# Kernel tuning notes

Measured on AMD Instinct MI355X. Metric: run time of the kernel, lower is better.

The kernel has to match this reference:

```python
import jax, jax.numpy as jnp
import numpy as np

B, N, NV, RESO, C_LAT = 1, 16384, 6890, 256, 192
C3 = C_LAT // 3            # 64 channels per uv/uh/hv plane
N_FREQ = 10                # NeRF PE -> 3*(2*10+1) = 63
UVH_DIM = 3 * (2 * N_FREQ + 1)
VIEW_DIM = 27
DEPTH_BOUND = 0.1
RGB_DIM = 3


def _embed(p):
    # p [B,N,3] -> [B,N,63]  (identity + sin/cos at 2^i freqs)
    freqs = (2.0 ** jnp.arange(N_FREQ)).astype(p.dtype)
    ang = p[..., None] * freqs                      # [B,N,3,F]
    s = jnp.sin(ang).reshape(p.shape[0], p.shape[1], -1)
    c = jnp.cos(ang).reshape(p.shape[0], p.shape[1], -1)
    return jnp.concatenate([p, s, c], axis=-1)


def _bilinear(plane, uv):
    # plane [B,C,H,W], uv [B,N,2] in [0,1] -> [B,C,N] (align_corners=True, border clamp)
    Bp, C, H, W = plane.shape
    x = jnp.clip(uv[..., 0], 0.0, 1.0) * (W - 1)
    y = jnp.clip(uv[..., 1], 0.0, 1.0) * (H - 1)
    x0 = jnp.floor(x); y0 = jnp.floor(y)
    wx = (x - x0)[:, None, :]; wy = (y - y0)[:, None, :]
    x0i = jnp.clip(x0.astype(jnp.int32), 0, W - 1)
    x1i = jnp.clip(x0i + 1, 0, W - 1)
    y0i = jnp.clip(y0.astype(jnp.int32), 0, H - 1)
    y1i = jnp.clip(y0i + 1, 0, H - 1)
    flat = plane.reshape(Bp, C, H * W)
    def g(yi, xi):
        idx = (yi * W + xi)[:, None, :]
        return jnp.take_along_axis(flat, jnp.broadcast_to(idx, (Bp, C, idx.shape[-1])), axis=2)
    f00 = g(y0i, x0i); f01 = g(y0i, x1i); f10 = g(y1i, x0i); f11 = g(y1i, x1i)
    return (f00 * (1 - wx) * (1 - wy) + f01 * wx * (1 - wy)
            + f10 * (1 - wx) * wy + f11 * wx * wy)


def _conv1d(x, w, b):
    # 1x1 Conv1d == channel matmul: x [B,Cin,N], w [Cout,Cin]
    return jnp.einsum('oc,bcn->bon', w, x) + b[None, :, None]


def _forward(sampled_pts, smpl_vertices, view_dir, input_latent, vts_uv,
             w_geo0, b_geo0, w_geo1, b_geo1, w_alpha, b_alpha,
             w_view0, b_view0, w_view1, b_view1, w_rgb, b_rgb):
    # --- KNN (k=1) nearest SMPL vertex via gram trick (no [B,N,V,3] diff) ---
    p2 = jnp.sum(sampled_pts ** 2, -1)                     # [B,N]
    v2 = jnp.sum(smpl_vertices ** 2, -1)                   # [B,V]
    d2 = (p2[:, :, None] + v2[:, None, :]
          - 2.0 * jnp.einsum('bnd,bvd->bnv', sampled_pts, smpl_vertices))  # [B,N,V]
    idx = jnp.argmin(d2, axis=-1)                          # [B,N]
    h = jnp.sqrt(jnp.maximum(jnp.min(d2, axis=-1), 1e-12))[..., None]      # [B,N,1]
    near_uv = vts_uv[0][idx]                               # [B,N,2]

    # --- uvh positional encoding (before depth normalization) ---
    pts_huv = jnp.concatenate([h, near_uv], axis=2)        # [B,N,3]
    huvlat = _embed(pts_huv).transpose(0, 2, 1)            # [B,63,N]

    # --- tri-plane (uv / uh / hv) grid-sample lookups ---
    h_n = (h / DEPTH_BOUND + 1.0) / 2.0
    uv_pl = input_latent[:, :C3]
    uh_pl = input_latent[:, C3:2 * C3]
    hv_pl = input_latent[:, 2 * C3:]
    uh = jnp.concatenate([near_uv[..., :1], h_n], -1)
    hv = jnp.concatenate([h_n, near_uv[..., 1:]], -1)
    fused = (_bilinear(uv_pl, near_uv) + _bilinear(uh_pl, uh) + _bilinear(hv_pl, hv)) / 3.0  # [B,64,N]

    # --- NeRF head (1x1 Conv1d MLP) ---
    nerf_in = jnp.concatenate([fused, huvlat], 1)          # [B,127,N]
    net = jax.nn.relu(_conv1d(nerf_in, w_geo0, b_geo0))
    net = jax.nn.relu(_conv1d(net, w_geo1, b_geo1))
    alpha = _conv1d(net, w_alpha, b_alpha)                 # [B,1,N]
    feat = jnp.concatenate([net, view_dir.transpose(0, 2, 1), fused], 1)   # [B,347,N]
    net = jax.nn.relu(_conv1d(feat, w_view0, b_view0))
    net = jax.nn.relu(_conv1d(net, w_view1, b_view1))
    rgb = _conv1d(net, w_rgb, b_rgb)                       # [B,3,N]
    return jnp.concatenate([alpha, rgb], 1).transpose(0, 2, 1)  # [B,N,4]


def setup_inputs():
    key = jax.random.key(0)
    ks = jax.random.split(key, 12)
    def rn(k, shape, scale=1.0):
        return (jax.random.normal(k, shape) * scale).astype(jnp.float32)
    return {
        'sampled_pts': rn(ks[0], (B, N, 3), 0.3),
        'smpl_vertices': rn(ks[1], (B, NV, 3), 0.3),
        'view_dir': rn(ks[2], (B, N, VIEW_DIM)),
        'input_latent': rn(ks[3], (B, C_LAT, RESO, RESO), 0.1),
        'vts_uv': jax.random.uniform(ks[4], (1, NV, 2), dtype=jnp.float32),
        'w_geo0': rn(ks[5], (256, C3 + UVH_DIM), 0.05), 'b_geo0': jnp.zeros(256),
        'w_geo1': rn(ks[6], (256, 256), 0.05), 'b_geo1': jnp.zeros(256),
        'w_alpha': rn(ks[7], (1, 256), 0.05), 'b_alpha': jnp.zeros(1),
        'w_view0': rn(ks[8], (256, 256 + VIEW_DIM + C3), 0.05), 'b_view0': jnp.zeros(256),
        'w_view1': rn(ks[9], (128, 256), 0.05), 'b_view1': jnp.zeros(128),
        'w_rgb': rn(ks[10], (RGB_DIM, 128), 0.05), 'b_rgb': jnp.zeros(RGB_DIM),
    }


def reference(sampled_pts, smpl_vertices, view_dir, input_latent, vts_uv,
              w_geo0, b_geo0, w_geo1, b_geo1, w_alpha, b_alpha,
              w_view0, b_view0, w_view1, b_view1, w_rgb, b_rgb):
    return _forward(sampled_pts, smpl_vertices, view_dir, input_latent, vts_uv,
                    w_geo0, b_geo0, w_geo1, b_geo1, w_alpha, b_alpha,
                    w_view0, b_view0, w_view1, b_view1, w_rgb, b_rgb)
```

## Files before the change

### kernel.cpp

```cpp
#include <hip/hip_runtime.h>
#include <hip/hip_bf16.h>
#include <math.h>
#include <float.h>

#define N_PTS 16384
#define NVERT 6890
#define RESO 256
#define C_LAT 192
#define VIEW_DIM 27

#define NCHUNK 16
#define CHUNK 431

typedef __hip_bfloat16 bf16;
typedef __bf16 bf16x8 __attribute__((ext_vector_type(8)));
typedef float f32x4 __attribute__((ext_vector_type(4)));

__device__ __forceinline__ void gload_lds16(const void* g, void* l) {
    __builtin_amdgcn_global_load_lds(
        (const __attribute__((address_space(1))) unsigned int*)g,
        (__attribute__((address_space(3))) unsigned int*)l, 16, 0, 0);
}

__global__ __launch_bounds__(256) void transpose_latent(const float* __restrict__ lat,
                                                        bf16* __restrict__ latT) {
    __shared__ float tile[C_LAT][65];
    int b = blockIdx.x;
    int y = b >> 2;
    int x0 = (b & 3) << 6;
    int t = threadIdx.x;
    #pragma unroll
    for (int i = 0; i < (C_LAT * 64) / 256; ++i) {
        int e = i * 256 + t;
        int c = e >> 6, xi = e & 63;
        tile[c][xi] = lat[c * (RESO * RESO) + y * RESO + x0 + xi];
    }
    __syncthreads();
    #pragma unroll
    for (int i = 0; i < (C_LAT * 64) / 256; ++i) {
        int e = i * 256 + t;
        int xi = e / C_LAT, c = e % C_LAT;
        latT[(size_t)(y * RESO + x0 + xi) * C_LAT + c] = __float2bfloat16(tile[c][xi]);
    }
}

__global__ __launch_bounds__(256) void nn_partial(const float* __restrict__ P,
                                                  const float* __restrict__ V,
                                                  float* __restrict__ pd2,
                                                  int* __restrict__ pidx) {
    __shared__ float4 vs[CHUNK];
    int t = threadIdx.x;
    int pc = blockIdx.x;
    int vc = blockIdx.y;
    int vstart = vc * CHUNK;
    int count = min(CHUNK, NVERT - vstart);
    for (int i = t; i < count; i += 256) {
        int g = vstart + i;
        float x = V[g * 3 + 0], y = V[g * 3 + 1], z = V[g * 3 + 2];
        float v2 = __fadd_rn(__fadd_rn(__fmul_rn(x, x), __fmul_rn(y, y)), __fmul_rn(z, z));
        vs[i] = make_float4(x, y, z, v2);
    }
    __syncthreads();
    int n = pc * 256 + t;
    float px = P[n * 3 + 0], py = P[n * 3 + 1], pz = P[n * 3 + 2];
    float p2 = __fadd_rn(__fadd_rn(__fmul_rn(px, px), __fmul_rn(py, py)), __fmul_rn(pz, pz));
    float best = FLT_MAX;
    int bi = 0;
    for (int v = 0; v < count; ++v) {
        float4 q = vs[v];
        float dot = fmaf(pz, q.z, fmaf(py, q.y, __fmul_rn(px, q.x)));
        float d2 = __fsub_rn(__fadd_rn(p2, q.w), __fmul_rn(2.0f, dot));
        if (d2 < best) { best = d2; bi = vstart + v; }
    }
    pd2[n * NCHUNK + vc] = best;
    pidx[n * NCHUNK + vc] = bi;
}

__global__ __launch_bounds__(256) void prep_weights(const float* __restrict__ w0,
                                                    const float* __restrict__ w1,
                                                    const float* __restrict__ w2,
                                                    const float* __restrict__ w3,
                                                    bf16* __restrict__ Wp0,
                                                    bf16* __restrict__ W1b,
                                                    bf16* __restrict__ Wp2,
                                                    bf16* __restrict__ W3b) {
    int i = blockIdx.x * 256 + threadIdx.x;
    if (i < 256 * 128) {
        int nn = i >> 7, k = i & 127;
        Wp0[i] = __float2bfloat16((k < 127) ? w0[nn * 127 + k] : 0.0f);
    }
    if (i < 256 * 256) {
        W1b[i] = __float2bfloat16(w1[i]);
    }
    if (i < 256 * 352) {
        int nn = i / 352, k = i % 352;
        Wp2[i] = __float2bfloat16((k < 347) ? w2[nn * 347 + k] : 0.0f);
    }
    if (i < 128 * 256) {
        W3b[i] = __float2bfloat16(w3[i]);
    }
}

__global__ __launch_bounds__(256) void sample_embed(const float* __restrict__ pd2,
                                                    const int* __restrict__ pidx,
                                                    const float* __restrict__ vts_uv,
                                                    const bf16* __restrict__ latT,
                                                    const float* __restrict__ view_dir,
                                                    bf16* __restrict__ X1,
                                                    bf16* __restrict__ X2) {
    int t = threadIdx.x;
    int lane = t & 63, w = t >> 6;
    int n = blockIdx.x * 4 + w;
    float best = FLT_MAX;
    int bi = 0;
    #pragma unroll
    for (int c = 0; c < NCHUNK; ++c) {
        float d = pd2[n * NCHUNK + c];
        int ix = pidx[n * NCHUNK + c];
        if (d < best) { best = d; bi = ix; }
    }
    float u = vts_uv[bi * 2 + 0], vv = vts_uv[bi * 2 + 1];
    float h = __fsqrt_rn(fmaxf(best, 1e-12f));
    float hn = __fmul_rn(__fadd_rn(__fdiv_rn(h, 0.1f), 1.0f), 0.5f);

    float fsum = 0.0f;
    #pragma unroll
    for (int p = 0; p < 3; ++p) {
        float xc = (p == 2) ? hn : u;
        float yc = (p == 1) ? hn : vv;
        float x = fminf(fmaxf(xc, 0.0f), 1.0f) * 255.0f;
        float y = fminf(fmaxf(yc, 0.0f), 1.0f) * 255.0f;
        float x0 = floorf(x), y0 = floorf(y);
        float wx = x - x0, wy = y - y0;
        int x0i = min(max((int)x0, 0), 255), y0i = min(max((int)y0, 0), 255);
        int x1i = min(x0i + 1, 255), y1i = min(y0i + 1, 255);
        int co = p * 64 + lane;
        float f00 = __bfloat162float(latT[(size_t)(y0i * 256 + x0i) * C_LAT + co]);
        float f01 = __bfloat162float(latT[(size_t)(y0i * 256 + x1i) * C_LAT + co]);
        float f10 = __bfloat162float(latT[(size_t)(y1i * 256 + x0i) * C_LAT + co]);
        float f11 = __bfloat162float(latT[(size_t)(y1i * 256 + x1i) * C_LAT + co]);
        fsum += f00 * (1 - wx) * (1 - wy) + f01 * wx * (1 - wy) + f10 * (1 - wx) * wy + f11 * wx * wy;
    }
    float fused = fsum / 3.0f;
    X1[(size_t)n * 128 + lane] = __float2bfloat16(fused);
    X2[(size_t)n * 352 + 283 + lane] = __float2bfloat16(fused);

    if (lane < 63) {
        float val;
        if (lane < 3) {
            val = (lane == 0) ? h : ((lane == 1) ? u : vv);
        } else {
            int e = lane - 3;
            if (e < 30) {
                int d = e / 10, k = e % 10;
                float pv = (d == 0) ? h : ((d == 1) ? u : vv);
                val = sinf(pv * (float)(1 << k));
            } else {
                e -= 30;
                int d = e / 10, k = e % 10;
                float pv = (d == 0) ? h : ((d == 1) ? u : vv);
                val = cosf(pv * (float)(1 << k));
            }
        }
        X1[(size_t)n * 128 + 64 + lane] = __float2bfloat16(val);
    } else {
        X1[(size_t)n * 128 + 127] = __float2bfloat16(0.0f);
    }
    if (lane < 27) {
        X2[(size_t)n * 352 + 256 + lane] = __float2bfloat16(view_dir[n * VIEW_DIM + lane]);
    } else if (lane < 32) {
        X2[(size_t)n * 352 + 347 + (lane - 27)] = __float2bfloat16(0.0f);
    }
}

template<int K, int LDX, int LDW, int LDY>
__global__ __launch_bounds__(256) void gemm_mfma(const bf16* __restrict__ X,
                                                 const bf16* __restrict__ W,
                                                 const float* __restrict__ bias,
                                                 bf16* __restrict__ Y) {
    __shared__ char smem[16384];
    const int t = threadIdx.x;
    const int bm = blockIdx.x, bn = blockIdx.y;
    const int l = t & 63, w = t >> 6;
    const int wr = w >> 1, wc = w & 1;
    const int lr = l & 15, lg = l >> 4;

    f32x4 acc[4][4];
    #pragma unroll
    for (int m = 0; m < 4; ++m)
        #pragma unroll
        for (int n = 0; n < 4; ++n) acc[m][n] = f32x4{0.f, 0.f, 0.f, 0.f};

    #pragma unroll
    for (int kt = 0; kt < K; kt += 32) {
        __syncthreads();
        #pragma unroll
        for (int i = 0; i < 2; ++i) {
            int p = i * 256 + t;
            int r = p >> 2, s = p & 3;
            int g = s ^ ((r >> 1) & 3);
            gload_lds16(X + (size_t)(bm * 128 + r) * LDX + kt + g * 8, smem + p * 16);
        }
        #pragma unroll
        for (int i = 0; i < 2; ++i) {
            int p = i * 256 + t;
            int r = p >> 2, s = p & 3;
            int g = s ^ ((r >> 1) & 3);
            gload_lds16(W + (size_t)(bn * 128 + r) * LDW + kt + g * 8, smem + 8192 + p * 16);
        }
        __syncthreads();
        bf16x8 af[4], bw[4];
        #pragma unroll
        for (int m = 0; m < 4; ++m) {
            int rr = wr * 64 + m * 16 + lr;
            int slot = lg ^ ((rr >> 1) & 3);
            af[m] = *(const bf16x8*)(smem + rr * 64 + slot * 16);
        }
        #pragma unroll
        for (int n = 0; n < 4; ++n) {
            int rr = wc * 64 + n * 16 + lr;
            int slot = lg ^ ((rr >> 1) & 3);
            bw[n] = *(const bf16x8*)(smem + 8192 + rr * 64 + slot * 16);
        }
        #pragma unroll
        for (int m = 0; m < 4; ++m)
            #pragma unroll
            for (int n = 0; n < 4; ++n)
                acc[m][n] = __builtin_amdgcn_mfma_f32_16x16x32_bf16(af[m], bw[n], acc[m][n], 0, 0, 0);
    }

    #pragma unroll
    for (int n = 0; n < 4; ++n) {
        int col = bn * 128 + wc * 64 + n * 16 + lr;
        float bv = bias[col];
        #pragma unroll
        for (int m = 0; m < 4; ++m) {
            int row0 = bm * 128 + wr * 64 + m * 16 + lg * 4;
            #pragma unroll
            for (int j = 0; j < 4; ++j) {
                float o = fmaxf(acc[m][n][j] + bv, 0.0f);
                Y[(size_t)(row0 + j) * LDY + col] = __float2bfloat16(o);
            }
        }
    }
}

__global__ __launch_bounds__(256) void finalize(const bf16* __restrict__ X2,
                                                const bf16* __restrict__ A4,
                                                const float* __restrict__ w_alpha,
                                                const float* __restrict__ b_alpha,
                                                const float* __restrict__ w_rgb,
                                                const float* __restrict__ b_rgb,
                                                float* __restrict__ out) {
    int t = threadIdx.x;
    int lane = t & 63, w = t >> 6;
    int n = blockIdx.x * 4 + w;
    float sa = 0.0f;
    #pragma unroll
    for (int i = 0; i < 4; ++i)
        sa = fmaf(__bfloat162float(X2[(size_t)n * 352 + lane + 64 * i]), w_alpha[lane + 64 * i], sa);
    float sr = 0.0f, sg = 0.0f, sb = 0.0f;
    #pragma unroll
    for (int i = 0; i < 2; ++i) {
        float a4 = __bfloat162float(A4[(size_t)n * 128 + lane + 64 * i]);
        sr = fmaf(a4, w_rgb[0 * 128 + lane + 64 * i], sr);
        sg = fmaf(a4, w_rgb[1 * 128 + lane + 64 * i], sg);
        sb = fmaf(a4, w_rgb[2 * 128 + lane + 64 * i], sb);
    }
    #pragma unroll
    for (int off = 32; off; off >>= 1) {
        sa += __shfl_xor(sa, off, 64);
        sr += __shfl_xor(sr, off, 64);
        sg += __shfl_xor(sg, off, 64);
        sb += __shfl_xor(sb, off, 64);
    }
    if (lane == 0) {
        out[(size_t)n * 4 + 0] = sa + b_alpha[0];
        out[(size_t)n * 4 + 1] = sr + b_rgb[0];
        out[(size_t)n * 4 + 2] = sg + b_rgb[1];
        out[(size_t)n * 4 + 3] = sb + b_rgb[2];
    }
}

extern "C" void kernel_launch(void* const* d_in, const int* in_sizes, int n_in,
                              void* d_out, int out_size, void* d_ws, size_t ws_size,
                              hipStream_t stream) {
    (void)in_sizes; (void)n_in; (void)out_size; (void)ws_size;
    const float* sampled_pts  = (const float*)d_in[0];
    const float* smpl_verts   = (const float*)d_in[1];
    const float* view_dir     = (const float*)d_in[2];
    const float* input_latent = (const float*)d_in[3];
    const float* vts_uv       = (const float*)d_in[4];
    const float* w_geo0 = (const float*)d_in[5];
    const float* b_geo0 = (const float*)d_in[6];
    const float* w_geo1 = (const float*)d_in[7];
    const float* b_geo1 = (const float*)d_in[8];
    const float* w_alpha = (const float*)d_in[9];
    const float* b_alpha = (const float*)d_in[10];
    const float* w_view0 = (const float*)d_in[11];
    const float* b_view0 = (const float*)d_in[12];
    const float* w_view1 = (const float*)d_in[13];
    const float* b_view1 = (const float*)d_in[14];
    const float* w_rgb = (const float*)d_in[15];
    const float* b_rgb = (const float*)d_in[16];

    char* ws = (char*)d_ws;
    size_t off = 0;
    auto alloc = [&](size_t bytes) { void* p = ws + off; off += (bytes + 255) & ~(size_t)255; return p; };
    bf16* latT = (bf16*)alloc((size_t)C_LAT * RESO * RESO * 2);
    float* pd2 = (float*)alloc((size_t)N_PTS * NCHUNK * 4);
    int*   pidx = (int*)alloc((size_t)N_PTS * NCHUNK * 4);
    bf16* X1 = (bf16*)alloc((size_t)N_PTS * 128 * 2);
    bf16* A1 = (bf16*)alloc((size_t)N_PTS * 256 * 2);
    bf16* X2 = (bf16*)alloc((size_t)N_PTS * 352 * 2);
    bf16* Wp0 = (bf16*)alloc((size_t)256 * 128 * 2);
    bf16* W1b = (bf16*)alloc((size_t)256 * 256 * 2);
    bf16* Wp2 = (bf16*)alloc((size_t)256 * 352 * 2);
    bf16* W3b = (bf16*)alloc((size_t)128 * 256 * 2);
    bf16* A3 = A1;
    bf16* A4 = X1;

    float* out = (float*)d_out;

    hipLaunchKernelGGL(transpose_latent, dim3(1024), dim3(256), 0, stream, input_latent, latT);
    hipLaunchKernelGGL(nn_partial, dim3(64, 16), dim3(256), 0, stream,
                       sampled_pts, smpl_verts, pd2, pidx);
    hipLaunchKernelGGL(prep_weights, dim3(352), dim3(256), 0, stream,
                       w_geo0, w_geo1, w_view0, w_view1, Wp0, W1b, Wp2, W3b);
    hipLaunchKernelGGL(sample_embed, dim3(4096), dim3(256), 0, stream,
                       pd2, pidx, vts_uv, latT, view_dir, X1, X2);
    hipLaunchKernelGGL((gemm_mfma<128, 128, 128, 256>), dim3(N_PTS / 128, 2), dim3(256), 0, stream,
                       X1, Wp0, b_geo0, A1);
    hipLaunchKernelGGL((gemm_mfma<256, 256, 256, 352>), dim3(N_PTS / 128, 2), dim3(256), 0, stream,
                       A1, W1b, b_geo1, X2);
    hipLaunchKernelGGL((gemm_mfma<352, 352, 352, 256>), dim3(N_PTS / 128, 2), dim3(256), 0, stream,
                       X2, Wp2, b_view0, A3);
    hipLaunchKernelGGL((gemm_mfma<256, 256, 256, 128>), dim3(N_PTS / 128, 1), dim3(256), 0, stream,
                       A3, W3b, b_view1, A4);
    hipLaunchKernelGGL(finalize, dim3(4096), dim3(256), 0, stream,
                       X2, A4, w_alpha, b_alpha, w_rgb, b_rgb, out);
}
```

Measured before the change: 200.5 us.

## Fuse KNN, sampling, MLP layers and head into one per-tile mega kernel

Replaces the separate nearest-vertex, sampling/embedding, four GEMM and finalize kernels with a single 512-thread kernel. Each block handles 64 points: it runs the KNN search over vertex slices per wave, does the bilinear sampling and embedding, and chains all MLP layers through swizzled LDS buffers, with weights read straight from global memory. This removes the global round trips for intermediate activations and cuts the kernel launch count. In exchange, each block now scans all 6890 vertices for only 64 points, weights are no longer staged or reused through LDS, and only 256 blocks are launched, which may leave GPU occupancy low.

```diff
diff --git a/kernel.cpp b/kernel.cpp
--- a/kernel.cpp
+++ b/kernel.cpp
@@ -8,19 +8,11 @@
 #define RESO 256
 #define C_LAT 192
 #define VIEW_DIM 27
-
-#define NCHUNK 16
-#define CHUNK 431
+#define ROWS 64
 
 typedef __hip_bfloat16 bf16;
 typedef __bf16 bf16x8 __attribute__((ext_vector_type(8)));
 typedef float f32x4 __attribute__((ext_vector_type(4)));
-
-__device__ __forceinline__ void gload_lds16(const void* g, void* l) {
-    __builtin_amdgcn_global_load_lds(
-        (const __attribute__((address_space(1))) unsigned int*)g,
-        (__attribute__((address_space(3))) unsigned int*)l, 16, 0, 0);
-}
 
 __global__ __launch_bounds__(256) void transpose_latent(const float* __restrict__ lat,
                                                         bf16* __restrict__ latT) {
@@ -44,241 +36,354 @@
     }
 }
 
-__global__ __launch_bounds__(256) void nn_partial(const float* __restrict__ P,
-                                                  const float* __restrict__ V,
-                                                  float* __restrict__ pd2,
-                                                  int* __restrict__ pidx) {
-    __shared__ float4 vs[CHUNK];
-    int t = threadIdx.x;
-    int pc = blockIdx.x;
-    int vc = blockIdx.y;
-    int vstart = vc * CHUNK;
-    int count = min(CHUNK, NVERT - vstart);
-    for (int i = t; i < count; i += 256) {
-        int g = vstart + i;
-        float x = V[g * 3 + 0], y = V[g * 3 + 1], z = V[g * 3 + 2];
-        float v2 = __fadd_rn(__fadd_rn(__fmul_rn(x, x), __fmul_rn(y, y)), __fmul_rn(z, z));
-        vs[i] = make_float4(x, y, z, v2);
-    }
-    __syncthreads();
-    int n = pc * 256 + t;
-    float px = P[n * 3 + 0], py = P[n * 3 + 1], pz = P[n * 3 + 2];
-    float p2 = __fadd_rn(__fadd_rn(__fmul_rn(px, px), __fmul_rn(py, py)), __fmul_rn(pz, pz));
-    float best = FLT_MAX;
-    int bi = 0;
-    for (int v = 0; v < count; ++v) {
-        float4 q = vs[v];
-        float dot = fmaf(pz, q.z, fmaf(py, q.y, __fmul_rn(px, q.x)));
-        float d2 = __fsub_rn(__fadd_rn(p2, q.w), __fmul_rn(2.0f, dot));
-        if (d2 < best) { best = d2; bi = vstart + v; }
-    }
-    pd2[n * NCHUNK + vc] = best;
-    pidx[n * NCHUNK + vc] = bi;
-}
-
-__global__ __launch_bounds__(256) void prep_weights(const float* __restrict__ w0,
-                                                    const float* __restrict__ w1,
-                                                    const float* __restrict__ w2,
-                                                    const float* __restrict__ w3,
-                                                    bf16* __restrict__ Wp0,
-                                                    bf16* __restrict__ W1b,
-                                                    bf16* __restrict__ Wp2,
-                                                    bf16* __restrict__ W3b) {
+__global__ __launch_bounds__(256) void prep(const float* __restrict__ w0,
+                                            const float* __restrict__ w1,
+                                            const float* __restrict__ w2,
+                                            const float* __restrict__ w3,
+                                            const float* __restrict__ V,
+                                            bf16* __restrict__ W0b,
+                                            bf16* __restrict__ W1b,
+                                            bf16* __restrict__ W2b,
+                                            bf16* __restrict__ W3b,
+                                            float4* __restrict__ V4) {
     int i = blockIdx.x * 256 + threadIdx.x;
     if (i < 256 * 128) {
-        int nn = i >> 7, k = i & 127;
-        Wp0[i] = __float2bfloat16((k < 127) ? w0[nn * 127 + k] : 0.0f);
-    }
-    if (i < 256 * 256) {
-        W1b[i] = __float2bfloat16(w1[i]);
-    }
-    if (i < 256 * 352) {
-        int nn = i / 352, k = i % 352;
-        Wp2[i] = __float2bfloat16((k < 347) ? w2[nn * 347 + k] : 0.0f);
-    }
-    if (i < 128 * 256) {
-        W3b[i] = __float2bfloat16(w3[i]);
+        int n = i >> 7, k = i & 127;
+        W0b[i] = __float2bfloat16((k < 127) ? w0[n * 127 + k] : 0.0f);
+    }
+    if (i < 256 * 256) W1b[i] = __float2bfloat16(w1[i]);
+    if (i < 256 * 384) {
+        int n = i / 384, k = i % 384;
+        W2b[i] = __float2bfloat16((k < 347) ? w2[n * 347 + k] : 0.0f);
+    }
+    if (i < 128 * 256) W3b[i] = __float2bfloat16(w3[i]);
+    if (i < NVERT) {
+        float x = V[i * 3 + 0], y = V[i * 3 + 1], z = V[i * 3 + 2];
+        float v2 = __fadd_rn(__fadd_rn(__fmul_rn(x, x), __fmul_rn(y, y)), __fmul_rn(z, z));
+        V4[i] = make_float4(x, y, z, v2);
     }
 }
 
-__global__ __launch_bounds__(256) void sample_embed(const float* __restrict__ pd2,
-                                                    const int* __restrict__ pidx,
-                                                    const float* __restrict__ vts_uv,
-                                                    const bf16* __restrict__ latT,
-                                                    const float* __restrict__ view_dir,
-                                                    bf16* __restrict__ X1,
-                                                    bf16* __restrict__ X2) {
-    int t = threadIdx.x;
-    int lane = t & 63, w = t >> 6;
-    int n = blockIdx.x * 4 + w;
-    float best = FLT_MAX;
-    int bi = 0;
-    #pragma unroll
-    for (int c = 0; c < NCHUNK; ++c) {
-        float d = pd2[n * NCHUNK + c];
-        int ix = pidx[n * NCHUNK + c];
-        if (d < best) { best = d; bi = ix; }
-    }
-    float u = vts_uv[bi * 2 + 0], vv = vts_uv[bi * 2 + 1];
-    float h = __fsqrt_rn(fmaxf(best, 1e-12f));
-    float hn = __fmul_rn(__fadd_rn(__fdiv_rn(h, 0.1f), 1.0f), 0.5f);
-
-    float fsum = 0.0f;
-    #pragma unroll
-    for (int p = 0; p < 3; ++p) {
-        float xc = (p == 2) ? hn : u;
-        float yc = (p == 1) ? hn : vv;
-        float x = fminf(fmaxf(xc, 0.0f), 1.0f) * 255.0f;
-        float y = fminf(fmaxf(yc, 0.0f), 1.0f) * 255.0f;
-        float x0 = floorf(x), y0 = floorf(y);
-        float wx = x - x0, wy = y - y0;
-        int x0i = min(max((int)x0, 0), 255), y0i = min(max((int)y0, 0), 255);
-        int x1i = min(x0i + 1, 255), y1i = min(y0i + 1, 255);
-        int co = p * 64 + lane;
-        float f00 = __bfloat162float(latT[(size_t)(y0i * 256 + x0i) * C_LAT + co]);
-        float f01 = __bfloat162float(latT[(size_t)(y0i * 256 + x1i) * C_LAT + co]);
-        float f10 = __bfloat162float(latT[(size_t)(y1i * 256 + x0i) * C_LAT + co]);
-        float f11 = __bfloat162float(latT[(size_t)(y1i * 256 + x1i) * C_LAT + co]);
-        fsum += f00 * (1 - wx) * (1 - wy) + f01 * wx * (1 - wy) + f10 * (1 - wx) * wy + f11 * wx * wy;
-    }
-    float fused = fsum / 3.0f;
-    X1[(size_t)n * 128 + lane] = __float2bfloat16(fused);
-    X2[(size_t)n * 352 + 283 + lane] = __float2bfloat16(fused);
-
-    if (lane < 63) {
-        float val;
-        if (lane < 3) {
-            val = (lane == 0) ? h : ((lane == 1) ? u : vv);
-        } else {
-            int e = lane - 3;
-            if (e < 30) {
+__device__ __forceinline__ int swz(int row, int kbyte, int LDB) {
+    return row * LDB + (kbyte ^ ((row & 7) << 4));
+}
+
+__global__ __launch_bounds__(512) void mega(const float* __restrict__ P,
+                                            const float4* __restrict__ V4,
+                                            const float* __restrict__ vts_uv,
+                                            const bf16* __restrict__ latT,
+                                            const float* __restrict__ view_dir,
+                                            const bf16* __restrict__ W0, const float* __restrict__ b0,
+                                            const bf16* __restrict__ W1, const float* __restrict__ b1,
+                                            const bf16* __restrict__ W2, const float* __restrict__ b2,
+                                            const bf16* __restrict__ W3, const float* __restrict__ b3,
+                                            const float* __restrict__ w_alpha, const float* __restrict__ b_alpha,
+                                            const float* __restrict__ w_rgb, const float* __restrict__ b_rgb,
+                                            float* __restrict__ out) {
+    __shared__ __align__(16) char bufA[ROWS * 512];
+    __shared__ __align__(16) char bufB[ROWS * 512];
+    __shared__ __align__(16) char bufC[ROWS * 256];
+    __shared__ float redF[8][ROWS];
+    __shared__ int   redI[8][ROWS];
+    __shared__ float hunv[3][ROWS];
+
+    const int t = threadIdx.x;
+    const int lane = t & 63;
+    const int w = t >> 6;
+    const int lr = lane & 15, lg = lane >> 4;
+    const int n0 = blockIdx.x * ROWS;
+
+    {
+        int wv = __builtin_amdgcn_readfirstlane(w);
+        int vstart = wv * 862;
+        int vend = min(vstart + 862, NVERT);
+        int n = n0 + lane;
+        float px = P[n * 3 + 0], py = P[n * 3 + 1], pz = P[n * 3 + 2];
+        float p2 = __fadd_rn(__fadd_rn(__fmul_rn(px, px), __fmul_rn(py, py)), __fmul_rn(pz, pz));
+        float best = FLT_MAX;
+        int bi = vstart;
+        #pragma unroll 4
+        for (int v = vstart; v < vend; ++v) {
+            float4 q = V4[v];
+            float dot = fmaf(pz, q.z, fmaf(py, q.y, __fmul_rn(px, q.x)));
+            float d2 = __fsub_rn(__fadd_rn(p2, q.w), __fmul_rn(2.0f, dot));
+            if (d2 < best) { best = d2; bi = v; }
+        }
+        redF[w][lane] = best;
+        redI[w][lane] = bi;
+    }
+    __syncthreads();
+    if (t < ROWS) {
+        float best = FLT_MAX;
+        int bi = 0;
+        #pragma unroll
+        for (int ww = 0; ww < 8; ++ww) {
+            float d = redF[ww][t];
+            int ix = redI[ww][t];
+            if (d < best) { best = d; bi = ix; }
+        }
+        hunv[0][t] = __fsqrt_rn(fmaxf(best, 1e-12f));
+        hunv[1][t] = vts_uv[bi * 2 + 0];
+        hunv[2][t] = vts_uv[bi * 2 + 1];
+    }
+    __syncthreads();
+
+    {
+        #pragma unroll
+        for (int pp = 0; pp < 8; ++pp) {
+            int p = w * 8 + pp;
+            float h = hunv[0][p], u = hunv[1][p], vv = hunv[2][p];
+            float hn = __fmul_rn(__fadd_rn(__fdiv_rn(h, 0.1f), 1.0f), 0.5f);
+            float fsum = 0.0f;
+            #pragma unroll
+            for (int pl = 0; pl < 3; ++pl) {
+                float xc = (pl == 2) ? hn : u;
+                float yc = (pl == 1) ? hn : vv;
+                float x = fminf(fmaxf(xc, 0.0f), 1.0f) * 255.0f;
+                float y = fminf(fmaxf(yc, 0.0f), 1.0f) * 255.0f;
+                float x0 = floorf(x), y0 = floorf(y);
+                float wx = x - x0, wy = y - y0;
+                int x0i = min(max((int)x0, 0), 255), y0i = min(max((int)y0, 0), 255);
+                int x1i = min(x0i + 1, 255), y1i = min(y0i + 1, 255);
+                int co = pl * 64 + lane;
+                float f00 = __bfloat162float(latT[(size_t)(y0i * 256 + x0i) * C_LAT + co]);
+                float f01 = __bfloat162float(latT[(size_t)(y0i * 256 + x1i) * C_LAT + co]);
+                float f10 = __bfloat162float(latT[(size_t)(y1i * 256 + x0i) * C_LAT + co]);
+                float f11 = __bfloat162float(latT[(size_t)(y1i * 256 + x1i) * C_LAT + co]);
+                fsum += f00 * (1 - wx) * (1 - wy) + f01 * wx * (1 - wy) + f10 * (1 - wx) * wy + f11 * wx * wy;
+            }
+            bf16 fb = __float2bfloat16(fsum / 3.0f);
+            *(bf16*)(bufA + swz(p, lane * 2, 256)) = fb;
+            *(bf16*)(bufC + swz(p, (27 + lane) * 2, 256)) = fb;
+        }
+    }
+
+    {
+        int p = t >> 3, i = t & 7;
+        float h = hunv[0][p], u = hunv[1][p], vv = hunv[2][p];
+        #pragma unroll
+        for (int r = 0; r < 8; ++r) {
+            int j = i + r * 8;
+            float val;
+            if (j == 63) {
+                val = 0.0f;
+            } else if (j < 3) {
+                val = (j == 0) ? h : ((j == 1) ? u : vv);
+            } else if (j < 33) {
+                int e = j - 3;
                 int d = e / 10, k = e % 10;
                 float pv = (d == 0) ? h : ((d == 1) ? u : vv);
                 val = sinf(pv * (float)(1 << k));
             } else {
-                e -= 30;
+                int e = j - 33;
                 int d = e / 10, k = e % 10;
                 float pv = (d == 0) ? h : ((d == 1) ? u : vv);
                 val = cosf(pv * (float)(1 << k));
             }
-        }
-        X1[(size_t)n * 128 + 64 + lane] = __float2bfloat16(val);
-    } else {
-        X1[(size_t)n * 128 + 127] = __float2bfloat16(0.0f);
-    }
-    if (lane < 27) {
-        X2[(size_t)n * 352 + 256 + lane] = __float2bfloat16(view_dir[n * VIEW_DIM + lane]);
-    } else if (lane < 32) {
-        X2[(size_t)n * 352 + 347 + (lane - 27)] = __float2bfloat16(0.0f);
-    }
-}
-
-template<int K, int LDX, int LDW, int LDY>
-__global__ __launch_bounds__(256) void gemm_mfma(const bf16* __restrict__ X,
-                                                 const bf16* __restrict__ W,
-                                                 const float* __restrict__ bias,
-                                                 bf16* __restrict__ Y) {
-    __shared__ char smem[16384];
-    const int t = threadIdx.x;
-    const int bm = blockIdx.x, bn = blockIdx.y;
-    const int l = t & 63, w = t >> 6;
-    const int wr = w >> 1, wc = w & 1;
-    const int lr = l & 15, lg = l >> 4;
-
-    f32x4 acc[4][4];
-    #pragma unroll
-    for (int m = 0; m < 4; ++m)
-        #pragma unroll
-        for (int n = 0; n < 4; ++n) acc[m][n] = f32x4{0.f, 0.f, 0.f, 0.f};
-
-    #pragma unroll
-    for (int kt = 0; kt < K; kt += 32) {
-        __syncthreads();
-        #pragma unroll
-        for (int i = 0; i < 2; ++i) {
-            int p = i * 256 + t;
-            int r = p >> 2, s = p & 3;
-            int g = s ^ ((r >> 1) & 3);
-            gload_lds16(X + (size_t)(bm * 128 + r) * LDX + kt + g * 8, smem + p * 16);
-        }
-        #pragma unroll
-        for (int i = 0; i < 2; ++i) {
-            int p = i * 256 + t;
-            int r = p >> 2, s = p & 3;
-            int g = s ^ ((r >> 1) & 3);
-            gload_lds16(W + (size_t)(bn * 128 + r) * LDW + kt + g * 8, smem + 8192 + p * 16);
-        }
-        __syncthreads();
-        bf16x8 af[4], bw[4];
-        #pragma unroll
-        for (int m = 0; m < 4; ++m) {
-            int rr = wr * 64 + m * 16 + lr;
-            int slot = lg ^ ((rr >> 1) & 3);
-            af[m] = *(const bf16x8*)(smem + rr * 64 + slot * 16);
-        }
-        #pragma unroll
-        for (int n = 0; n < 4; ++n) {
-            int rr = wc * 64 + n * 16 + lr;
-            int slot = lg ^ ((rr >> 1) & 3);
-            bw[n] = *(const bf16x8*)(smem + 8192 + rr * 64 + slot * 16);
-        }
-        #pragma unroll
-        for (int m = 0; m < 4; ++m)
-            #pragma unroll
-            for (int n = 0; n < 4; ++n)
-                acc[m][n] = __builtin_amdgcn_mfma_f32_16x16x32_bf16(af[m], bw[n], acc[m][n], 0, 0, 0);
-    }
-
-    #pragma unroll
-    for (int n = 0; n < 4; ++n) {
-        int col = bn * 128 + wc * 64 + n * 16 + lr;
-        float bv = bias[col];
-        #pragma unroll
-        for (int m = 0; m < 4; ++m) {
-            int row0 = bm * 128 + wr * 64 + m * 16 + lg * 4;
-            #pragma unroll
-            for (int j = 0; j < 4; ++j) {
-                float o = fmaxf(acc[m][n][j] + bv, 0.0f);
-                Y[(size_t)(row0 + j) * LDY + col] = __float2bfloat16(o);
-            }
-        }
-    }
-}
-
-__global__ __launch_bounds__(256) void finalize(const bf16* __restrict__ X2,
-                                                const bf16* __restrict__ A4,
-                                                const float* __restrict__ w_alpha,
-                                                const float* __restrict__ b_alpha,
-                                                const float* __restrict__ w_rgb,
-                                                const float* __restrict__ b_rgb,
-                                                float* __restrict__ out) {
-    int t = threadIdx.x;
-    int lane = t & 63, w = t >> 6;
-    int n = blockIdx.x * 4 + w;
-    float sa = 0.0f;
-    #pragma unroll
-    for (int i = 0; i < 4; ++i)
-        sa = fmaf(__bfloat162float(X2[(size_t)n * 352 + lane + 64 * i]), w_alpha[lane + 64 * i], sa);
-    float sr = 0.0f, sg = 0.0f, sb = 0.0f;
-    #pragma unroll
-    for (int i = 0; i < 2; ++i) {
-        float a4 = __bfloat162float(A4[(size_t)n * 128 + lane + 64 * i]);
-        sr = fmaf(a4, w_rgb[0 * 128 + lane + 64 * i], sr);
-        sg = fmaf(a4, w_rgb[1 * 128 + lane + 64 * i], sg);
-        sb = fmaf(a4, w_rgb[2 * 128 + lane + 64 * i], sb);
-    }
-    #pragma unroll
-    for (int off = 32; off; off >>= 1) {
-        sa += __shfl_xor(sa, off, 64);
-        sr += __shfl_xor(sr, off, 64);
-        sg += __shfl_xor(sg, off, 64);
-        sb += __shfl_xor(sb, off, 64);
-    }
-    if (lane == 0) {
-        out[(size_t)n * 4 + 0] = sa + b_alpha[0];
-        out[(size_t)n * 4 + 1] = sr + b_rgb[0];
-        out[(size_t)n * 4 + 2] = sg + b_rgb[1];
-        out[(size_t)n * 4 + 3] = sb + b_rgb[2];
+            *(bf16*)(bufA + swz(p, (64 + j) * 2, 256)) = __float2bfloat16(val);
+        }
+        #pragma unroll
+        for (int r = 0; r < 4; ++r) {
+            int c = i + r * 8;
+            if (c < VIEW_DIM)
+                *(bf16*)(bufC + swz(p, c * 2, 256)) =
+                    __float2bfloat16(view_dir[(size_t)(n0 + p) * VIEW_DIM + c]);
+        }
+        #pragma unroll
+        for (int r = 0; r < 5; ++r) {
+            int c = 91 + i + r * 8;
+            if (c < 128)
+                *(bf16*)(bufC + swz(p, c * 2, 256)) = __float2bfloat16(0.0f);
+        }
+    }
+    __syncthreads();
+
+    const int wm = w >> 2, wn = w & 3;
+
+    {
+        f32x4 acc[2][4] = {};
+        #pragma unroll
+        for (int ks = 0; ks < 4; ++ks) {
+            int kt = ks * 32;
+            bf16x8 a[2], b[4];
+            #pragma unroll
+            for (int m = 0; m < 2; ++m) {
+                int row = wm * 32 + m * 16 + lr;
+                a[m] = *(const bf16x8*)(bufA + swz(row, (kt + lg * 8) * 2, 256));
+            }
+            #pragma unroll
+            for (int nn = 0; nn < 4; ++nn) {
+                int col = wn * 64 + nn * 16 + lr;
+                b[nn] = *(const bf16x8*)(W0 + (size_t)col * 128 + kt + lg * 8);
+            }
+            #pragma unroll
+            for (int m = 0; m < 2; ++m)
+                #pragma unroll
+                for (int nn = 0; nn < 4; ++nn)
+                    acc[m][nn] = __builtin_amdgcn_mfma_f32_16x16x32_bf16(a[m], b[nn], acc[m][nn], 0, 0, 0);
+        }
+        #pragma unroll
+        for (int nn = 0; nn < 4; ++nn) {
+            int col = wn * 64 + nn * 16 + lr;
+            float bv = b0[col];
+            #pragma unroll
+            for (int m = 0; m < 2; ++m)
+                #pragma unroll
+                for (int j = 0; j < 4; ++j) {
+                    int row = wm * 32 + m * 16 + lg * 4 + j;
+                    *(bf16*)(bufB + swz(row, col * 2, 512)) =
+                        __float2bfloat16(fmaxf(acc[m][nn][j] + bv, 0.0f));
+                }
+        }
+    }
+    __syncthreads();
+
+    {
+        f32x4 acc[2][4] = {};
+        #pragma unroll
+        for (int ks = 0; ks < 8; ++ks) {
+            int kt = ks * 32;
+            bf16x8 a[2], b[4];
+            #pragma unroll
+            for (int m = 0; m < 2; ++m) {
+                int row = wm * 32 + m * 16 + lr;
+                a[m] = *(const bf16x8*)(bufB + swz(row, (kt + lg * 8) * 2, 512));
+            }
+            #pragma unroll
+            for (int nn = 0; nn < 4; ++nn) {
+                int col = wn * 64 + nn * 16 + lr;
+                b[nn] = *(const bf16x8*)(W1 + (size_t)col * 256 + kt + lg * 8);
+            }
+            #pragma unroll
+            for (int m = 0; m < 2; ++m)
+                #pragma unroll
+                for (int nn = 0; nn < 4; ++nn)
+                    acc[m][nn] = __builtin_amdgcn_mfma_f32_16x16x32_bf16(a[m], b[nn], acc[m][nn], 0, 0, 0);
+        }
+        #pragma unroll
+        for (int nn = 0; nn < 4; ++nn) {
+            int col = wn * 64 + nn * 16 + lr;
+            float bv = b1[col];
+            #pragma unroll
+            for (int m = 0; m < 2; ++m)
+                #pragma unroll
+                for (int j = 0; j < 4; ++j) {
+                    int row = wm * 32 + m * 16 + lg * 4 + j;
+                    *(bf16*)(bufA + swz(row, col * 2, 512)) =
+                        __float2bfloat16(fmaxf(acc[m][nn][j] + bv, 0.0f));
+                }
+        }
+    }
+    __syncthreads();
+
+    {
+        f32x4 acc[2][4] = {};
+        #pragma unroll
+        for (int ks = 0; ks < 12; ++ks) {
+            int kt = ks * 32;
+            bf16x8 a[2], b[4];
+            #pragma unroll
+            for (int m = 0; m < 2; ++m) {
+                int row = wm * 32 + m * 16 + lr;
+                if (kt < 256)
+                    a[m] = *(const bf16x8*)(bufA + swz(row, (kt + lg * 8) * 2, 512));
+                else
+                    a[m] = *(const bf16x8*)(bufC + swz(row, (kt - 256 + lg * 8) * 2, 256));
+            }
+            #pragma unroll
+            for (int nn = 0; nn < 4; ++nn) {
+                int col = wn * 64 + nn * 16 + lr;
+                b[nn] = *(const bf16x8*)(W2 + (size_t)col * 384 + kt + lg * 8);
+            }
+            #pragma unroll
+            for (int m = 0; m < 2; ++m)
+                #pragma unroll
+                for (int nn = 0; nn < 4; ++nn)
+                    acc[m][nn] = __builtin_amdgcn_mfma_f32_16x16x32_bf16(a[m], b[nn], acc[m][nn], 0, 0, 0);
+        }
+        #pragma unroll
+        for (int nn = 0; nn < 4; ++nn) {
+            int col = wn * 64 + nn * 16 + lr;
+            float bv = b2[col];
+            #pragma unroll
+            for (int m = 0; m < 2; ++m)
+                #pragma unroll
+                for (int j = 0; j < 4; ++j) {
+                    int row = wm * 32 + m * 16 + lg * 4 + j;
+                    *(bf16*)(bufB + swz(row, col * 2, 512)) =
+                        __float2bfloat16(fmaxf(acc[m][nn][j] + bv, 0.0f));
+                }
+        }
+    }
+    __syncthreads();
+
+    {
+        f32x4 acc[2][2] = {};
+        #pragma unroll
+        for (int ks = 0; ks < 8; ++ks) {
+            int kt = ks * 32;
+            bf16x8 a[2], b[2];
+            #pragma unroll
+            for (int m = 0; m < 2; ++m) {
+                int row = wm * 32 + m * 16 + lr;
+                a[m] = *(const bf16x8*)(bufB + swz(row, (kt + lg * 8) * 2, 512));
+            }
+            #pragma unroll
+            for (int nn = 0; nn < 2; ++nn) {
+                int col = wn * 32 + nn * 16 + lr;
+                b[nn] = *(const bf16x8*)(W3 + (size_t)col * 256 + kt + lg * 8);
+            }
+            #pragma unroll
+            for (int m = 0; m < 2; ++m)
+                #pragma unroll
+                for (int nn = 0; nn < 2; ++nn)
+                    acc[m][nn] = __builtin_amdgcn_mfma_f32_16x16x32_bf16(a[m], b[nn], acc[m][nn], 0, 0, 0);
+        }
+        #pragma unroll
+        for (int nn = 0; nn < 2; ++nn) {
+            int col = wn * 32 + nn * 16 + lr;
+            float bv = b3[col];
+            #pragma unroll
+            for (int m = 0; m < 2; ++m)
+                #pragma unroll
+                for (int j = 0; j < 4; ++j) {
+                    int row = wm * 32 + m * 16 + lg * 4 + j;
+                    *(bf16*)(bufC + swz(row, col * 2, 256)) =
+                        __float2bfloat16(fmaxf(acc[m][nn][j] + bv, 0.0f));
+                }
+        }
+    }
+    __syncthreads();
+
+    {
+        int p = t >> 3, g = t & 7;
+        float sa = 0.0f;
+        #pragma unroll
+        for (int c0 = 0; c0 < 32; ++c0) {
+            int col = g * 32 + c0;
+            float x = __bfloat162float(*(const bf16*)(bufA + swz(p, col * 2, 512)));
+            sa = fmaf(x, w_alpha[col], sa);
+        }
+        float sr = 0.0f, sg = 0.0f, sb = 0.0f;
+        #pragma unroll
+        for (int c0 = 0; c0 < 16; ++c0) {
+            int col = g * 16 + c0;
+            float x = __bfloat162float(*(const bf16*)(bufC + swz(p, col * 2, 256)));
+            sr = fmaf(x, w_rgb[0 * 128 + col], sr);
+            sg = fmaf(x, w_rgb[1 * 128 + col], sg);
+            sb = fmaf(x, w_rgb[2 * 128 + col], sb);
+        }
+        #pragma unroll
+        for (int off = 4; off; off >>= 1) {
+            sa += __shfl_xor(sa, off, 64);
+            sr += __shfl_xor(sr, off, 64);
+            sg += __shfl_xor(sg, off, 64);
+            sb += __shfl_xor(sb, off, 64);
+        }
+        if (g == 0) {
+            float4 o = make_float4(sa + b_alpha[0], sr + b_rgb[0], sg + b_rgb[1], sb + b_rgb[2]);
+            *(float4*)(out + (size_t)(n0 + p) * 4) = o;
+        }
     }
 }
 
@@ -307,36 +412,21 @@
     char* ws = (char*)d_ws;
     size_t off = 0;
     auto alloc = [&](size_t bytes) { void* p = ws + off; off += (bytes + 255) & ~(size_t)255; return p; };
-    bf16* latT = (bf16*)alloc((size_t)C_LAT * RESO * RESO * 2);
-    float* pd2 = (float*)alloc((size_t)N_PTS * NCHUNK * 4);
-    int*   pidx = (int*)alloc((size_t)N_PTS * NCHUNK * 4);
-    bf16* X1 = (bf16*)alloc((size_t)N_PTS * 128 * 2);
-    bf16* A1 = (bf16*)alloc((size_t)N_PTS * 256 * 2);
-    bf16* X2 = (bf16*)alloc((size_t)N_PTS * 352 * 2);
-    bf16* Wp0 = (bf16*)alloc((size_t)256 * 128 * 2);
-    bf16* W1b = (bf16*)alloc((size_t)256 * 256 * 2);
-    bf16* Wp2 = (bf16*)alloc((size_t)256 * 352 * 2);
-    bf16* W3b = (bf16*)alloc((size_t)128 * 256 * 2);
-    bf16* A3 = A1;
-    bf16* A4 = X1;
+    bf16*   latT = (bf16*)alloc((size_t)C_LAT * RESO * RESO * 2);
+    float4* V4   = (float4*)alloc((size_t)NVERT * 16);
+    bf16*   W0b  = (bf16*)alloc((size_t)256 * 128 * 2);
+    bf16*   W1b  = (bf16*)alloc((size_t)256 * 256 * 2);
+    bf16*   W2b  = (bf16*)alloc((size_t)256 * 384 * 2);
+    bf16*   W3b  = (bf16*)alloc((size_t)128 * 256 * 2);
 
     float* out = (float*)d_out;
 
     hipLaunchKernelGGL(transpose_latent, dim3(1024), dim3(256), 0, stream, input_latent, latT);
-    hipLaunchKernelGGL(nn_partial, dim3(64, 16), dim3(256), 0, stream,
-                       sampled_pts, smpl_verts, pd2, pidx);
-    hipLaunchKernelGGL(prep_weights, dim3(352), dim3(256), 0, stream,
-                       w_geo0, w_geo1, w_view0, w_view1, Wp0, W1b, Wp2, W3b);
-    hipLaunchKernelGGL(sample_embed, dim3(4096), dim3(256), 0, stream,
-                       pd2, pidx, vts_uv, latT, view_dir, X1, X2);
-    hipLaunchKernelGGL((gemm_mfma<128, 128, 128, 256>), dim3(N_PTS / 128, 2), dim3(256), 0, stream,
-                       X1, Wp0, b_geo0, A1);
-    hipLaunchKernelGGL((gemm_mfma<256, 256, 256, 352>), dim3(N_PTS / 128, 2), dim3(256), 0, stream,
-                       A1, W1b, b_geo1, X2);
-    hipLaunchKernelGGL((gemm_mfma<352, 352, 352, 256>), dim3(N_PTS / 128, 2), dim3(256), 0, stream,
-                       X2, Wp2, b_view0, A3);
-    hipLaunchKernelGGL((gemm_mfma<256, 256, 256, 128>), dim3(N_PTS / 128, 1), dim3(256), 0, stream,
-                       A3, W3b, b_view1, A4);
-    hipLaunchKernelGGL(finalize, dim3(4096), dim3(256), 0, stream,
-                       X2, A4, w_alpha, b_alpha, w_rgb, b_rgb, out);
+    hipLaunchKernelGGL(prep, dim3(384), dim3(256), 0, stream,
+                       w_geo0, w_geo1, w_view0, w_view1, smpl_verts,
+                       W0b, W1b, W2b, W3b, V4);
+    hipLaunchKernelGGL(mega, dim3(N_PTS / ROWS), dim3(512), 0, stream,
+                       sampled_pts, V4, vts_uv, latT, view_dir,
+                       W0b, b_geo0, W1b, b_geo1, W2b, b_view0, W3b, b_view1,
+                       w_alpha, b_alpha, w_rgb, b_rgb, out);
 }
```

Result: slower. 240.1 us (+19.7%).
